# Kernel optimization log

Hardware: AMD Instinct MI355X
Metric: run time of the kernel (lower is better)

## Reference

```python
import jax, jax.numpy as jnp
import numpy as np

H = 256  # hidden_channels
N_USERS = 100000
N_MOVIES = 50000
N_EDGES = 500000


def setup_inputs() -> dict:
    key = jax.random.key(0)
    k1, k2, k3, k4, k5, k6, k7 = jax.random.split(key, 7)
    user_emb = jax.random.normal(k1, (N_USERS, H), dtype=jnp.float32)
    movie_emb = jax.random.normal(k2, (N_MOVIES, H), dtype=jnp.float32)
    edge_label_index = jax.random.randint(k3, (2, N_EDGES), 0, N_MOVIES, dtype=jnp.int64)
    # Linear(2H, H) and Linear(H, 1) params, torch default init scale
    s1 = 1.0 / np.sqrt(2 * H)
    s2 = 1.0 / np.sqrt(H)
    W1 = jax.random.uniform(k4, (2 * H, H), dtype=jnp.float32, minval=-s1, maxval=s1)
    b1 = jax.random.uniform(k5, (H,), dtype=jnp.float32, minval=-s1, maxval=s1)
    W2 = jax.random.uniform(k6, (H, 1), dtype=jnp.float32, minval=-s2, maxval=s2)
    b2 = jax.random.uniform(k7, (1,), dtype=jnp.float32, minval=-s2, maxval=s2)
    return {"user_emb": user_emb, "movie_emb": movie_emb,
            "edge_label_index": edge_label_index,
            "W1": W1, "b1": b1, "W2": W2, "b2": b2}


def reference(user_emb, movie_emb, edge_label_index, W1, b1, W2, b2):
    u = user_emb[edge_label_index[0]]    # [E, H]
    m = movie_emb[edge_label_index[1]]   # [E, H]
    x = jnp.concatenate([u, m], axis=-1)  # [E, 2H]
    x = jax.nn.relu(x @ W1 + b1)          # [E, H]
    return x @ W2 + b2                    # [E, 1]
```

## Files before the change

kernel.cpp:

```cpp
#include <hip/hip_runtime.h>
#include <hip/hip_bf16.h>

typedef __attribute__((ext_vector_type(8))) short v8s;
typedef __attribute__((ext_vector_type(4))) float v4f;

constexpr int H  = 256;
constexpr int K2 = 512;
constexpr int XS = 72;
constexpr int WS = 72;

__device__ inline unsigned short f2bf(float f) {
    unsigned int u = __builtin_bit_cast(unsigned int, f);
    u += 0x7FFFu + ((u >> 16) & 1u);
    return (unsigned short)(u >> 16);
}
__device__ inline float bf2f(unsigned short s) {
    return __builtin_bit_cast(float, (unsigned int)s << 16);
}

#define BAR_LGKM() do {                                          \
    asm volatile("s_waitcnt lgkmcnt(0)" ::: "memory");           \
    __builtin_amdgcn_sched_barrier(0);                           \
    __builtin_amdgcn_s_barrier();                                \
    __builtin_amdgcn_sched_barrier(0);                           \
} while (0)

__global__ void w1_transpose_kernel(const float* __restrict__ w1,
                                    unsigned short* __restrict__ w1t) {
    __shared__ float tile[32][33];
    const int bk = blockIdx.x;
    const int bn = blockIdx.y;
    const int tx = threadIdx.x & 31;
    const int ty8 = threadIdx.x >> 5;
#pragma unroll
    for (int i = 0; i < 4; ++i) {
        int ty = i * 8 + ty8;
        tile[ty][tx] = w1[(size_t)(bk * 32 + ty) * H + bn * 32 + tx];
    }
    __syncthreads();
#pragma unroll
    for (int i = 0; i < 4; ++i) {
        int ty = i * 8 + ty8;
        w1t[(size_t)(bn * 32 + ty) * K2 + bk * 32 + tx] = f2bf(tile[tx][ty]);
    }
}

__global__ void flag_zero_kernel(unsigned char* __restrict__ f, const int n) {
    int i = threadIdx.x + blockIdx.x * blockDim.x;
    int stride = blockDim.x * gridDim.x;
    for (; i < n; i += stride) f[i] = 0;
}

__global__ void flag_fill_kernel(const int* __restrict__ eli,
                                 unsigned char* __restrict__ fu,
                                 unsigned char* __restrict__ fm,
                                 const int E, const int nu, const int nm) {
    const long stride = (long)blockDim.x * gridDim.x;
    for (long e = threadIdx.x + (long)blockIdx.x * blockDim.x; e < E; e += stride) {
        int u = eli[e];
        int m = eli[(long)E + e];
        u = u < 0 ? 0 : (u >= nu ? nu - 1 : u);
        m = m < 0 ? 0 : (m >= nm ? nm - 1 : m);
        fu[u >> 6] = 1;
        fm[m >> 6] = 1;
    }
}

__global__ __launch_bounds__(512, 2) void emb_gemm_persist_kernel(
    const float* __restrict__ user_emb,
    const float* __restrict__ movie_emb,
    const unsigned short* __restrict__ w1t,
    const float* __restrict__ b1,
    unsigned short* __restrict__ P,
    unsigned short* __restrict__ Q,
    const int n_users, const int n_movies,
    const unsigned char* __restrict__ fu,
    const unsigned char* __restrict__ fm)
{
    __shared__ __align__(16) unsigned short Xs[64 * 256];
    __shared__ int list[64];
    __shared__ int nact_s;

    const int bid   = blockIdx.x;
    const int nside = (int)(gridDim.x >> 1);
    const int isMovie = bid & 1;
    const int base  = bid >> 1;

    const float* emb = isMovie ? movie_emb : user_emb;
    unsigned short* outp = isMovie ? Q : P;
    const int M    = isMovie ? n_movies : n_users;
    const int kofs = isMovie ? 256 : 0;
    const int nch  = (M + 63) >> 6;
    const unsigned char* flags = isMovie ? fm : fu;

    const int t    = threadIdx.x;
    const int wave = t >> 6;
    const int lane = t & 63;
    const int wm   = wave >> 2;
    const int wn   = wave & 3;
    const int quad = lane >> 4;
    const int l16  = lane & 15;

    if (wave == 0) {
        int c = base + lane * nside;
        bool a = (c < nch) && (flags[c] != 0);
        unsigned long long mk = __ballot(a);
        if (a) list[__popcll(mk & ((1ull << lane) - 1ull))] = c;
        if (lane == 0) nact_s = (int)__popcll(mk);
    }
    __syncthreads();
    const int nact = nact_s;
    if (nact == 0) return;

    v8s B[4][4][2];
    {
        const unsigned short* wb = w1t + (size_t)(wn * 64 + l16) * K2 + kofs + quad * 8;
#pragma unroll
        for (int nt = 0; nt < 4; ++nt)
#pragma unroll
            for (int kt = 0; kt < 4; ++kt)
#pragma unroll
                for (int ks = 0; ks < 2; ++ks)
                    B[nt][kt][ks] = *(const v8s*)(wb + (size_t)nt * 16 * K2 + kt * 64 + ks * 32);
    }
    float bv[4];
#pragma unroll
    for (int nt = 0; nt < 4; ++nt)
        bv[nt] = isMovie ? 0.f : b1[wn * 64 + nt * 16 + l16];

    char* const xsb = (char*)Xs;
    v4f xq[8];

    auto LOADX = [&](int c) {
#pragma unroll
        for (int i = 0; i < 8; ++i) {
            long r = (long)c * 64 + wave * 8 + i;
            if (r >= M) r = M - 1;
            xq[i] = *(const v4f*)(emb + (size_t)r * H + lane * 4);
        }
    };
    auto WRITEX = [&]() {
#pragma unroll
        for (int i = 0; i < 8; ++i) {
            const int r = wave * 8 + i;
            unsigned int lo = (unsigned)f2bf(xq[i][0]) | ((unsigned)f2bf(xq[i][1]) << 16);
            unsigned int hi = (unsigned)f2bf(xq[i][2]) | ((unsigned)f2bf(xq[i][3]) << 16);
            *(unsigned long long*)(xsb + r * 512 + ((lane * 8) ^ (i << 4))) =
                ((unsigned long long)hi << 32) | lo;
        }
    };

    LOADX(list[0]);
    WRITEX();
    if (nact > 1) LOADX(list[1]);
    __syncthreads();

    for (int j = 0; j < nact; ++j) {
        const long m0 = (long)list[j] * 64;

        v4f acc[2][4];
#pragma unroll
        for (int mt = 0; mt < 2; ++mt)
#pragma unroll
            for (int nt = 0; nt < 4; ++nt)
                acc[mt][nt] = (v4f){0.f, 0.f, 0.f, 0.f};

#pragma unroll
        for (int kt = 0; kt < 4; ++kt)
#pragma unroll
            for (int ks = 0; ks < 2; ++ks) {
                v8s af[2];
#pragma unroll
                for (int mt = 0; mt < 2; ++mt) {
                    const int row = wm * 32 + mt * 16 + l16;
                    af[mt] = *(const v8s*)(xsb + row * 512 +
                        ((kt * 128 + ks * 64 + quad * 16) ^ ((l16 & 7) << 4)));
                }
#pragma unroll
                for (int mt = 0; mt < 2; ++mt)
#pragma unroll
                    for (int nt = 0; nt < 4; ++nt)
                        acc[mt][nt] = __builtin_amdgcn_mfma_f32_16x16x32_bf16(
                            af[mt], B[nt][kt][ks], acc[mt][nt], 0, 0, 0);
            }

#pragma unroll
        for (int mt = 0; mt < 2; ++mt)
#pragma unroll
            for (int j4 = 0; j4 < 4; ++j4) {
                const long m = m0 + wm * 32 + mt * 16 + quad * 4 + j4;
                if (m < M) {
#pragma unroll
                    for (int nt = 0; nt < 4; ++nt)
                        outp[(size_t)m * H + wn * 64 + nt * 16 + l16] =
                            f2bf(acc[mt][nt][j4] + bv[nt]);
                }
            }

        if (j + 1 < nact) {
            BAR_LGKM();
            WRITEX();
            if (j + 2 < nact) LOADX(list[j + 2]);
            BAR_LGKM();
        }
    }
}

__global__ __launch_bounds__(256, 8) void edge_score_kernel(
    const unsigned short* __restrict__ P,
    const unsigned short* __restrict__ Q,
    const int* __restrict__ eli,
    const float* __restrict__ w2,
    const float* __restrict__ b2,
    float* __restrict__ out,
    const int E, const int n_users, const int n_movies)
{
    const int t   = threadIdx.x;
    const int hw  = t >> 5;
    const int l32 = t & 31;

    float w2v[8];
    {
        v4f a = *(const v4f*)(w2 + l32 * 8);
        v4f b = *(const v4f*)(w2 + l32 * 8 + 4);
#pragma unroll
        for (int i = 0; i < 4; ++i) { w2v[i] = a[i]; w2v[4 + i] = b[i]; }
    }
    const float b2v = b2[0];
    const long base = (long)blockIdx.x * 64;

    int us[8], ms[8];
#pragma unroll
    for (int i = 0; i < 8; ++i) {
        long e = base + i * 8 + hw;
        long ec = (e < E) ? e : 0;
        int u = eli[ec];
        int m = eli[(long)E + ec];
        us[i] = u < 0 ? 0 : (u >= n_users  ? n_users  - 1 : u);
        ms[i] = m < 0 ? 0 : (m >= n_movies ? n_movies - 1 : m);
    }

    v8s pv = *(const v8s*)(P + (size_t)us[0] * H + l32 * 8);
    v8s qv = *(const v8s*)(Q + (size_t)ms[0] * H + l32 * 8);

#pragma unroll
    for (int i = 0; i < 8; ++i) {
        v8s pn, qn;
        if (i < 7) {
            pn = *(const v8s*)(P + (size_t)us[i + 1] * H + l32 * 8);
            qn = *(const v8s*)(Q + (size_t)ms[i + 1] * H + l32 * 8);
        }
        float s = 0.f;
#pragma unroll
        for (int j = 0; j < 8; ++j) {
            float h = bf2f((unsigned short)pv[j]) + bf2f((unsigned short)qv[j]);
            h = h > 0.f ? h : 0.f;
            s += h * w2v[j];
        }
        s += __shfl_xor(s, 1, 64);
        s += __shfl_xor(s, 2, 64);
        s += __shfl_xor(s, 4, 64);
        s += __shfl_xor(s, 8, 64);
        s += __shfl_xor(s, 16, 64);
        long e = base + i * 8 + hw;
        if (l32 == 0 && e < E) out[e] = s + b2v;
        pv = pn; qv = qn;
    }
}

constexpr int BMF = 64;
__global__ __launch_bounds__(512, 4) void edge_decoder_kernel(
    const float* __restrict__ user_emb, const float* __restrict__ movie_emb,
    const int* __restrict__ eli, const unsigned short* __restrict__ w1t,
    const float* __restrict__ b1, const float* __restrict__ w2,
    const float* __restrict__ b2, float* __restrict__ out,
    const int E, const int n_users, const int n_movies)
{
    __shared__ unsigned short Xs[BMF * XS];
    __shared__ unsigned short Wts[H * WS];
    __shared__ float red[4][BMF];
    const int t = threadIdx.x, wave = t >> 6, lane = t & 63;
    const int wm = wave >> 2, wn = wave & 3, quad = lane >> 4, l16 = lane & 15;
    const long e0 = (long)blockIdx.x * BMF;
    const int xr = t >> 3, xc = t & 7;
    long eg = e0 + xr; if (eg >= E) eg = 0;
    int iu = eli[eg], im = eli[(long)E + eg];
    iu = iu < 0 ? 0 : (iu >= n_users ? n_users - 1 : iu);
    im = im < 0 ? 0 : (im >= n_movies ? n_movies - 1 : im);
    const float* urow = user_emb + (size_t)iu * H;
    const float* mrow = movie_emb + (size_t)im * H;
    const int wr = t >> 3, wc8 = t & 7;
    const unsigned short* wbase = w1t + (size_t)wr * K2 + wc8 * 8;
    v4f acc[2][4];
#pragma unroll
    for (int mt = 0; mt < 2; ++mt)
#pragma unroll
        for (int nt = 0; nt < 4; ++nt) acc[mt][nt] = (v4f){0.f,0.f,0.f,0.f};
    v4f xq0 = *(const v4f*)(urow + xc * 8);
    v4f xq1 = *(const v4f*)(urow + xc * 8 + 4);
    v8s wq[4];
#pragma unroll
    for (int j = 0; j < 4; ++j) wq[j] = *(const v8s*)(wbase + (size_t)j * 64 * K2);
    for (int kt = 0; kt < 8; ++kt) {
        __syncthreads();
        { v8s xv;
#pragma unroll
          for (int i = 0; i < 4; ++i) xv[i] = (short)f2bf(xq0[i]);
#pragma unroll
          for (int i = 0; i < 4; ++i) xv[4+i] = (short)f2bf(xq1[i]);
          *(v8s*)(Xs + xr * XS + xc * 8) = xv; }
#pragma unroll
        for (int j = 0; j < 4; ++j) *(v8s*)(Wts + (j * 64 + wr) * WS + wc8 * 8) = wq[j];
        if (kt < 7) {
            const int kn = kt + 1, koff = (kn * 64) & 255;
            const float* src = ((kn < 4) ? urow : mrow) + koff + xc * 8;
            xq0 = *(const v4f*)(src); xq1 = *(const v4f*)(src + 4);
#pragma unroll
            for (int j = 0; j < 4; ++j) wq[j] = *(const v8s*)(wbase + (size_t)j * 64 * K2 + kn * 64);
        }
        __syncthreads();
#pragma unroll
        for (int ks = 0; ks < 2; ++ks) {
            v8s af[2], bf[4];
#pragma unroll
            for (int mt = 0; mt < 2; ++mt)
                af[mt] = *(const v8s*)(Xs + (wm * 32 + mt * 16 + l16) * XS + ks * 32 + quad * 8);
#pragma unroll
            for (int nt = 0; nt < 4; ++nt)
                bf[nt] = *(const v8s*)(Wts + (wn * 64 + nt * 16 + l16) * WS + ks * 32 + quad * 8);
#pragma unroll
            for (int mt = 0; mt < 2; ++mt)
#pragma unroll
                for (int nt = 0; nt < 4; ++nt)
                    acc[mt][nt] = __builtin_amdgcn_mfma_f32_16x16x32_bf16(af[mt], bf[nt], acc[mt][nt], 0, 0, 0);
        }
    }
    float b1v[4], w2v[4];
#pragma unroll
    for (int nt = 0; nt < 4; ++nt) {
        int n = wn * 64 + nt * 16 + l16;
        b1v[nt] = b1[n]; w2v[nt] = w2[n];
    }
    const float b2v = b2[0];
#pragma unroll
    for (int mt = 0; mt < 2; ++mt) {
        float s[4] = {0.f,0.f,0.f,0.f};
#pragma unroll
        for (int nt = 0; nt < 4; ++nt)
#pragma unroll
            for (int j = 0; j < 4; ++j) {
                float h = acc[mt][nt][j] + b1v[nt];
                h = h > 0.f ? h : 0.f;
                s[j] += h * w2v[nt];
            }
#pragma unroll
        for (int j = 0; j < 4; ++j) {
            float v = s[j];
            v += __shfl_xor(v, 1, 64); v += __shfl_xor(v, 2, 64);
            v += __shfl_xor(v, 4, 64); v += __shfl_xor(v, 8, 64);
            if (l16 == 0) red[wn][wm * 32 + mt * 16 + quad * 4 + j] = v;
        }
    }
    __syncthreads();
    if (t < BMF) {
        long e = e0 + t;
        if (e < E) out[e] = red[0][t] + red[1][t] + red[2][t] + red[3][t] + b2v;
    }
}

extern "C" void kernel_launch(void* const* d_in, const int* in_sizes, int n_in,
                              void* d_out, int out_size, void* d_ws, size_t ws_size,
                              hipStream_t stream) {
    const float* user_emb  = (const float*)d_in[0];
    const float* movie_emb = (const float*)d_in[1];
    const int*   eli       = (const int*)d_in[2];
    const float* w1        = (const float*)d_in[3];
    const float* b1        = (const float*)d_in[4];
    const float* w2        = (const float*)d_in[5];
    const float* b2        = (const float*)d_in[6];
    float*       out       = (float*)d_out;

    const int E        = out_size;
    const int n_users  = in_sizes[0] / H;
    const int n_movies = in_sizes[1] / H;

    unsigned short* w1t = (unsigned short*)d_ws;
    const size_t w1t_bytes = (size_t)K2 * H * 2;
    const size_t p_bytes   = (size_t)n_users  * H * 2;
    const size_t q_bytes   = (size_t)n_movies * H * 2;

    const int nbu = (n_users  + 63) / 64;
    const int nbm = (n_movies + 63) / 64;
    const size_t flag_bytes = (size_t)nbu + (size_t)nbm;

    w1_transpose_kernel<<<dim3(16, 8), 256, 0, stream>>>(w1, w1t);

    if (ws_size >= w1t_bytes + p_bytes + q_bytes + flag_bytes &&
        nbu <= 64 * 128 && nbm <= 64 * 128) {
        unsigned short* P = (unsigned short*)((char*)d_ws + w1t_bytes);
        unsigned short* Q = (unsigned short*)((char*)d_ws + w1t_bytes + p_bytes);
        unsigned char*  fu = (unsigned char*)((char*)d_ws + w1t_bytes + p_bytes + q_bytes);
        unsigned char*  fm = fu + nbu;

        flag_zero_kernel<<<4, 256, 0, stream>>>(fu, nbu + nbm);
        if (E > 0)
            flag_fill_kernel<<<512, 256, 0, stream>>>(eli, fu, fm, E, n_users, n_movies);
        emb_gemm_persist_kernel<<<256, 512, 0, stream>>>(
            user_emb, movie_emb, w1t, b1, P, Q, n_users, n_movies, fu, fm);
        if (E > 0)
            edge_score_kernel<<<(E + 63) / 64, 256, 0, stream>>>(
                P, Q, eli, w2, b2, out, E, n_users, n_movies);
    } else {
        if (E > 0)
            edge_decoder_kernel<<<(E + BMF - 1) / BMF, 512, 0, stream>>>(
                user_emb, movie_emb, eli, w1t, b1, w2, b2, out, E, n_users, n_movies);
    }
}
```

Before: 263.7 us.

## Stage W1 tile in LDS and double threads per GEMM block; fuse flag zeroing

```diff
diff --git a/kernel.cpp b/kernel.cpp
--- a/kernel.cpp
+++ b/kernel.cpp
@@ -26,12 +26,17 @@
 } while (0)
 
 __global__ void w1_transpose_kernel(const float* __restrict__ w1,
-                                    unsigned short* __restrict__ w1t) {
+                                    unsigned short* __restrict__ w1t,
+                                    unsigned char* __restrict__ flags,
+                                    const int nflags) {
     __shared__ float tile[32][33];
     const int bk = blockIdx.x;
     const int bn = blockIdx.y;
     const int tx = threadIdx.x & 31;
     const int ty8 = threadIdx.x >> 5;
+    if (flags && bk == 0 && bn == 0) {
+        for (int i = threadIdx.x; i < nflags; i += 256) flags[i] = 0;
+    }
 #pragma unroll
     for (int i = 0; i < 4; ++i) {
         int ty = i * 8 + ty8;
@@ -43,12 +48,6 @@
         int ty = i * 8 + ty8;
         w1t[(size_t)(bn * 32 + ty) * K2 + bk * 32 + tx] = f2bf(tile[tx][ty]);
     }
-}
-
-__global__ void flag_zero_kernel(unsigned char* __restrict__ f, const int n) {
-    int i = threadIdx.x + blockIdx.x * blockDim.x;
-    int stride = blockDim.x * gridDim.x;
-    for (; i < n; i += stride) f[i] = 0;
 }
 
 __global__ void flag_fill_kernel(const int* __restrict__ eli,
@@ -66,7 +65,7 @@
     }
 }
 
-__global__ __launch_bounds__(512, 2) void emb_gemm_persist_kernel(
+__global__ __launch_bounds__(1024, 4) void emb_gemm_persist_kernel(
     const float* __restrict__ user_emb,
     const float* __restrict__ movie_emb,
     const unsigned short* __restrict__ w1t,
@@ -77,9 +76,8 @@
     const unsigned char* __restrict__ fu,
     const unsigned char* __restrict__ fm)
 {
+    __shared__ __align__(16) unsigned short Bs[256 * 256];
     __shared__ __align__(16) unsigned short Xs[64 * 256];
-    __shared__ int list[64];
-    __shared__ int nact_s;
 
     const int bid   = blockIdx.x;
     const int nside = (int)(gridDim.x >> 1);
@@ -100,107 +98,112 @@
     const int wn   = wave & 3;
     const int quad = lane >> 4;
     const int l16  = lane & 15;
-
-    if (wave == 0) {
+    (void)wave;
+
+    unsigned long long mk;
+    {
         int c = base + lane * nside;
         bool a = (c < nch) && (flags[c] != 0);
-        unsigned long long mk = __ballot(a);
-        if (a) list[__popcll(mk & ((1ull << lane) - 1ull))] = c;
-        if (lane == 0) nact_s = (int)__popcll(mk);
-    }
-    __syncthreads();
-    const int nact = nact_s;
+        mk = __ballot(a);
+    }
+    const int nact = (int)__popcll(mk);
     if (nact == 0) return;
 
-    v8s B[4][4][2];
+    unsigned long long cur = mk, pf = mk;
+    auto nextc = [&](unsigned long long& m) -> int {
+        int p = (int)__builtin_ctzll(m);
+        m &= m - 1;
+        return base + p * nside;
+    };
+
+    char* const bsb = (char*)Bs;
+    char* const xsb = (char*)Xs;
+
     {
-        const unsigned short* wb = w1t + (size_t)(wn * 64 + l16) * K2 + kofs + quad * 8;
-#pragma unroll
-        for (int nt = 0; nt < 4; ++nt)
-#pragma unroll
-            for (int kt = 0; kt < 4; ++kt)
-#pragma unroll
-                for (int ks = 0; ks < 2; ++ks)
-                    B[nt][kt][ks] = *(const v8s*)(wb + (size_t)nt * 16 * K2 + kt * 64 + ks * 32);
-    }
+        const int n0 = t >> 5;
+        const int k8 = t & 31;
+#pragma unroll
+        for (int p = 0; p < 8; ++p) {
+            const int n = p * 32 + n0;
+            v8s w = *(const v8s*)(w1t + (size_t)n * K2 + kofs + k8 * 8);
+            *(v8s*)(bsb + n * 512 + ((k8 * 16) ^ ((n & 7) << 4))) = w;
+        }
+    }
+
     float bv[4];
 #pragma unroll
     for (int nt = 0; nt < 4; ++nt)
         bv[nt] = isMovie ? 0.f : b1[wn * 64 + nt * 16 + l16];
 
-    char* const xsb = (char*)Xs;
-    v4f xq[8];
+    const int xr = t >> 4;
+    const int xc = t & 15;
+    v4f xq[4];
 
     auto LOADX = [&](int c) {
-#pragma unroll
-        for (int i = 0; i < 8; ++i) {
-            long r = (long)c * 64 + wave * 8 + i;
-            if (r >= M) r = M - 1;
-            xq[i] = *(const v4f*)(emb + (size_t)r * H + lane * 4);
-        }
+        long r = (long)c * 64 + xr;
+        if (r >= M) r = M - 1;
+        const float* src = emb + (size_t)r * H + xc * 4;
+#pragma unroll
+        for (int q = 0; q < 4; ++q)
+            xq[q] = *(const v4f*)(src + q * 64);
     };
     auto WRITEX = [&]() {
 #pragma unroll
-        for (int i = 0; i < 8; ++i) {
-            const int r = wave * 8 + i;
-            unsigned int lo = (unsigned)f2bf(xq[i][0]) | ((unsigned)f2bf(xq[i][1]) << 16);
-            unsigned int hi = (unsigned)f2bf(xq[i][2]) | ((unsigned)f2bf(xq[i][3]) << 16);
-            *(unsigned long long*)(xsb + r * 512 + ((lane * 8) ^ (i << 4))) =
+        for (int q = 0; q < 4; ++q) {
+            unsigned int lo = (unsigned)f2bf(xq[q][0]) | ((unsigned)f2bf(xq[q][1]) << 16);
+            unsigned int hi = (unsigned)f2bf(xq[q][2]) | ((unsigned)f2bf(xq[q][3]) << 16);
+            *(unsigned long long*)(xsb + xr * 512 + ((xc * 8 + q * 128) ^ ((xr & 7) << 4))) =
                 ((unsigned long long)hi << 32) | lo;
         }
     };
 
-    LOADX(list[0]);
+    LOADX(nextc(pf));
     WRITEX();
-    if (nact > 1) LOADX(list[1]);
+    if (nact > 1) LOADX(nextc(pf));
     __syncthreads();
 
     for (int j = 0; j < nact; ++j) {
-        const long m0 = (long)list[j] * 64;
-
-        v4f acc[2][4];
-#pragma unroll
-        for (int mt = 0; mt < 2; ++mt)
-#pragma unroll
-            for (int nt = 0; nt < 4; ++nt)
-                acc[mt][nt] = (v4f){0.f, 0.f, 0.f, 0.f};
+        const long m0 = (long)nextc(cur) * 64;
+
+        v4f acc[4];
+#pragma unroll
+        for (int nt = 0; nt < 4; ++nt)
+            acc[nt] = (v4f){0.f, 0.f, 0.f, 0.f};
 
 #pragma unroll
         for (int kt = 0; kt < 4; ++kt)
 #pragma unroll
             for (int ks = 0; ks < 2; ++ks) {
-                v8s af[2];
-#pragma unroll
-                for (int mt = 0; mt < 2; ++mt) {
-                    const int row = wm * 32 + mt * 16 + l16;
-                    af[mt] = *(const v8s*)(xsb + row * 512 +
-                        ((kt * 128 + ks * 64 + quad * 16) ^ ((l16 & 7) << 4)));
+                const int ko = (kt * 128 + ks * 64 + quad * 16) ^ ((l16 & 7) << 4);
+                const int row = wm * 16 + l16;
+                v8s af = *(const v8s*)(xsb + row * 512 + ko);
+                v8s bf[4];
+#pragma unroll
+                for (int nt = 0; nt < 4; ++nt) {
+                    const int nn = wn * 64 + nt * 16 + l16;
+                    bf[nt] = *(const v8s*)(bsb + nn * 512 + ko);
                 }
 #pragma unroll
-                for (int mt = 0; mt < 2; ++mt)
-#pragma unroll
-                    for (int nt = 0; nt < 4; ++nt)
-                        acc[mt][nt] = __builtin_amdgcn_mfma_f32_16x16x32_bf16(
-                            af[mt], B[nt][kt][ks], acc[mt][nt], 0, 0, 0);
+                for (int nt = 0; nt < 4; ++nt)
+                    acc[nt] = __builtin_amdgcn_mfma_f32_16x16x32_bf16(
+                        af, bf[nt], acc[nt], 0, 0, 0);
             }
 
 #pragma unroll
-        for (int mt = 0; mt < 2; ++mt)
-#pragma unroll
-            for (int j4 = 0; j4 < 4; ++j4) {
-                const long m = m0 + wm * 32 + mt * 16 + quad * 4 + j4;
-                if (m < M) {
-#pragma unroll
-                    for (int nt = 0; nt < 4; ++nt)
-                        outp[(size_t)m * H + wn * 64 + nt * 16 + l16] =
-                            f2bf(acc[mt][nt][j4] + bv[nt]);
-                }
+        for (int j4 = 0; j4 < 4; ++j4) {
+            const long m = m0 + wm * 16 + quad * 4 + j4;
+            if (m < M) {
+#pragma unroll
+                for (int nt = 0; nt < 4; ++nt)
+                    outp[(size_t)m * H + wn * 64 + nt * 16 + l16] =
+                        f2bf(acc[nt][j4] + bv[nt]);
             }
+        }
 
         if (j + 1 < nact) {
             BAR_LGKM();
             WRITEX();
-            if (j + 2 < nact) LOADX(list[j + 2]);
+            if (j + 2 < nact) LOADX(nextc(pf));
             BAR_LGKM();
         }
     }
@@ -393,8 +396,6 @@
     const int nbm = (n_movies + 63) / 64;
     const size_t flag_bytes = (size_t)nbu + (size_t)nbm;
 
-    w1_transpose_kernel<<<dim3(16, 8), 256, 0, stream>>>(w1, w1t);
-
     if (ws_size >= w1t_bytes + p_bytes + q_bytes + flag_bytes &&
         nbu <= 64 * 128 && nbm <= 64 * 128) {
         unsigned short* P = (unsigned short*)((char*)d_ws + w1t_bytes);
@@ -402,15 +403,16 @@
         unsigned char*  fu = (unsigned char*)((char*)d_ws + w1t_bytes + p_bytes + q_bytes);
         unsigned char*  fm = fu + nbu;
 
-        flag_zero_kernel<<<4, 256, 0, stream>>>(fu, nbu + nbm);
+        w1_transpose_kernel<<<dim3(16, 8), 256, 0, stream>>>(w1, w1t, fu, nbu + nbm);
         if (E > 0)
             flag_fill_kernel<<<512, 256, 0, stream>>>(eli, fu, fm, E, n_users, n_movies);
-        emb_gemm_persist_kernel<<<256, 512, 0, stream>>>(
+        emb_gemm_persist_kernel<<<256, 1024, 0, stream>>>(
             user_emb, movie_emb, w1t, b1, P, Q, n_users, n_movies, fu, fm);
         if (E > 0)
             edge_score_kernel<<<(E + 63) / 64, 256, 0, stream>>>(
                 P, Q, eli, w2, b2, out, E, n_users, n_movies);
     } else {
+        w1_transpose_kernel<<<dim3(16, 8), 256, 0, stream>>>(w1, w1t, nullptr, 0);
         if (E > 0)
             edge_decoder_kernel<<<(E + BMF - 1) / BMF, 512, 0, stream>>>(
                 user_emb, movie_emb, eli, w1t, b1, w2, b2, out, E, n_users, n_movies);
```

After: 268.2 us. Within noise of the previous version (+1.7%).

## Stage embeddings via async global-to-LDS loads with double buffering in persistent GEMM

Applied to the files above, without the earlier changes.

```diff
diff --git a/kernel.cpp b/kernel.cpp
--- a/kernel.cpp
+++ b/kernel.cpp
@@ -18,20 +18,21 @@
     return __builtin_bit_cast(float, (unsigned int)s << 16);
 }
 
-#define BAR_LGKM() do {                                          \
-    asm volatile("s_waitcnt lgkmcnt(0)" ::: "memory");           \
-    __builtin_amdgcn_sched_barrier(0);                           \
-    __builtin_amdgcn_s_barrier();                                \
-    __builtin_amdgcn_sched_barrier(0);                           \
-} while (0)
+#define SB() __builtin_amdgcn_sched_barrier(0)
+#define VMW(N) do { asm volatile("s_waitcnt vmcnt(" #N ")" ::: "memory"); SB(); } while (0)
 
 __global__ void w1_transpose_kernel(const float* __restrict__ w1,
-                                    unsigned short* __restrict__ w1t) {
+                                    unsigned short* __restrict__ w1t,
+                                    unsigned char* __restrict__ flags,
+                                    const int nflags) {
     __shared__ float tile[32][33];
     const int bk = blockIdx.x;
     const int bn = blockIdx.y;
     const int tx = threadIdx.x & 31;
     const int ty8 = threadIdx.x >> 5;
+    if (flags && bk == 0 && bn == 0) {
+        for (int i = threadIdx.x; i < nflags; i += 256) flags[i] = 0;
+    }
 #pragma unroll
     for (int i = 0; i < 4; ++i) {
         int ty = i * 8 + ty8;
@@ -43,12 +44,6 @@
         int ty = i * 8 + ty8;
         w1t[(size_t)(bn * 32 + ty) * K2 + bk * 32 + tx] = f2bf(tile[tx][ty]);
     }
-}
-
-__global__ void flag_zero_kernel(unsigned char* __restrict__ f, const int n) {
-    int i = threadIdx.x + blockIdx.x * blockDim.x;
-    int stride = blockDim.x * gridDim.x;
-    for (; i < n; i += stride) f[i] = 0;
 }
 
 __global__ void flag_fill_kernel(const int* __restrict__ eli,
@@ -77,9 +72,7 @@
     const unsigned char* __restrict__ fu,
     const unsigned char* __restrict__ fm)
 {
-    __shared__ __align__(16) unsigned short Xs[64 * 256];
-    __shared__ int list[64];
-    __shared__ int nact_s;
+    __shared__ __align__(16) char Xs[2][64][1024];
 
     const int bid   = blockIdx.x;
     const int nside = (int)(gridDim.x >> 1);
@@ -101,16 +94,21 @@
     const int quad = lane >> 4;
     const int l16  = lane & 15;
 
-    if (wave == 0) {
+    unsigned long long mk;
+    {
         int c = base + lane * nside;
         bool a = (c < nch) && (flags[c] != 0);
-        unsigned long long mk = __ballot(a);
-        if (a) list[__popcll(mk & ((1ull << lane) - 1ull))] = c;
-        if (lane == 0) nact_s = (int)__popcll(mk);
-    }
-    __syncthreads();
-    const int nact = nact_s;
+        mk = __ballot(a);
+    }
+    const int nact = (int)__popcll(mk);
     if (nact == 0) return;
+
+    unsigned long long cur = mk, pf = mk;
+    auto nextc = [&](unsigned long long& m) -> int {
+        int p = (int)__builtin_ctzll(m);
+        m &= m - 1;
+        return base + p * nside;
+    };
 
     v8s B[4][4][2];
     {
@@ -127,36 +125,33 @@
 #pragma unroll
     for (int nt = 0; nt < 4; ++nt)
         bv[nt] = isMovie ? 0.f : b1[wn * 64 + nt * 16 + l16];
-
-    char* const xsb = (char*)Xs;
-    v4f xq[8];
-
-    auto LOADX = [&](int c) {
+    SB();
+
+    auto STAGE = [&](int c, int b) {
 #pragma unroll
         for (int i = 0; i < 8; ++i) {
-            long r = (long)c * 64 + wave * 8 + i;
+            const int rl = wave * 8 + i;
+            long r = (long)c * 64 + rl;
             if (r >= M) r = M - 1;
-            xq[i] = *(const v4f*)(emb + (size_t)r * H + lane * 4);
-        }
+            const char* src = (const char*)(emb + (size_t)r * H) + ((lane * 16) ^ (i << 4));
+            __builtin_amdgcn_global_load_lds(
+                (const __attribute__((address_space(1))) unsigned int*)src,
+                (__attribute__((address_space(3))) unsigned int*)&Xs[b][rl][0],
+                16, 0, 0);
+        }
+        SB();
     };
-    auto WRITEX = [&]() {
-#pragma unroll
-        for (int i = 0; i < 8; ++i) {
-            const int r = wave * 8 + i;
-            unsigned int lo = (unsigned)f2bf(xq[i][0]) | ((unsigned)f2bf(xq[i][1]) << 16);
-            unsigned int hi = (unsigned)f2bf(xq[i][2]) | ((unsigned)f2bf(xq[i][3]) << 16);
-            *(unsigned long long*)(xsb + r * 512 + ((lane * 8) ^ (i << 4))) =
-                ((unsigned long long)hi << 32) | lo;
-        }
-    };
-
-    LOADX(list[0]);
-    WRITEX();
-    if (nact > 1) LOADX(list[1]);
-    __syncthreads();
+
+    STAGE(nextc(pf), 0);
+    if (nact > 1) STAGE(nextc(pf), 1);
 
     for (int j = 0; j < nact; ++j) {
-        const long m0 = (long)list[j] * 64;
+        const int cb = j & 1;
+        const long m0 = (long)nextc(cur) * 64;
+
+        if (j == 0) { if (nact > 1) VMW(8); else VMW(0); }
+        else        { if (j + 1 < nact) VMW(40); else VMW(32); }
+        __builtin_amdgcn_s_barrier(); SB();
 
         v4f acc[2][4];
 #pragma unroll
@@ -165,44 +160,46 @@
             for (int nt = 0; nt < 4; ++nt)
                 acc[mt][nt] = (v4f){0.f, 0.f, 0.f, 0.f};
 
-#pragma unroll
-        for (int kt = 0; kt < 4; ++kt)
-#pragma unroll
-            for (int ks = 0; ks < 2; ++ks) {
-                v8s af[2];
-#pragma unroll
-                for (int mt = 0; mt < 2; ++mt) {
-                    const int row = wm * 32 + mt * 16 + l16;
-                    af[mt] = *(const v8s*)(xsb + row * 512 +
-                        ((kt * 128 + ks * 64 + quad * 16) ^ ((l16 & 7) << 4)));
+        const char* xb = &Xs[cb][0][0];
+#pragma unroll
+        for (int kk = 0; kk < 8; ++kk) {
+            v8s af[2];
+#pragma unroll
+            for (int mt = 0; mt < 2; ++mt) {
+                const int row = wm * 32 + mt * 16 + l16;
+                const int sw  = (row & 7) << 4;
+                const char* pr = xb + row * 1024;
+                v4f f0 = *(const v4f*)(pr + ((kk * 128 + quad * 32) ^ sw));
+                v4f f1 = *(const v4f*)(pr + ((kk * 128 + quad * 32 + 16) ^ sw));
+                v8s a;
+#pragma unroll
+                for (int q2 = 0; q2 < 4; ++q2) {
+                    a[q2]     = (short)f2bf(f0[q2]);
+                    a[4 + q2] = (short)f2bf(f1[q2]);
                 }
-#pragma unroll
-                for (int mt = 0; mt < 2; ++mt)
-#pragma unroll
-                    for (int nt = 0; nt < 4; ++nt)
-                        acc[mt][nt] = __builtin_amdgcn_mfma_f32_16x16x32_bf16(
-                            af[mt], B[nt][kt][ks], acc[mt][nt], 0, 0, 0);
+                af[mt] = a;
             }
+#pragma unroll
+            for (int mt = 0; mt < 2; ++mt)
+#pragma unroll
+                for (int nt = 0; nt < 4; ++nt)
+                    acc[mt][nt] = __builtin_amdgcn_mfma_f32_16x16x32_bf16(
+                        af[mt], B[nt][kk >> 1][kk & 1], acc[mt][nt], 0, 0, 0);
+        }
 
 #pragma unroll
         for (int mt = 0; mt < 2; ++mt)
 #pragma unroll
             for (int j4 = 0; j4 < 4; ++j4) {
                 const long m = m0 + wm * 32 + mt * 16 + quad * 4 + j4;
-                if (m < M) {
-#pragma unroll
-                    for (int nt = 0; nt < 4; ++nt)
-                        outp[(size_t)m * H + wn * 64 + nt * 16 + l16] =
-                            f2bf(acc[mt][nt][j4] + bv[nt]);
-                }
+#pragma unroll
+                for (int nt = 0; nt < 4; ++nt)
+                    outp[(size_t)m * H + wn * 64 + nt * 16 + l16] =
+                        f2bf(acc[mt][nt][j4] + bv[nt]);
             }
-
-        if (j + 1 < nact) {
-            BAR_LGKM();
-            WRITEX();
-            if (j + 2 < nact) LOADX(list[j + 2]);
-            BAR_LGKM();
-        }
+        SB();
+        __builtin_amdgcn_s_barrier(); SB();
+        if (j + 2 < nact) STAGE(nextc(pf), cb);
     }
 }
 
@@ -213,7 +210,7 @@
     const float* __restrict__ w2,
     const float* __restrict__ b2,
     float* __restrict__ out,
-    const int E, const int n_users, const int n_movies)
+    const int E, const int n_users, const int n_movies, const long e0)
 {
     const int t   = threadIdx.x;
     const int hw  = t >> 5;
@@ -227,7 +224,7 @@
         for (int i = 0; i < 4; ++i) { w2v[i] = a[i]; w2v[4 + i] = b[i]; }
     }
     const float b2v = b2[0];
-    const long base = (long)blockIdx.x * 64;
+    const long base = e0 + (long)blockIdx.x * 64;
 
     int us[8], ms[8];
 #pragma unroll
@@ -386,14 +383,12 @@
 
     unsigned short* w1t = (unsigned short*)d_ws;
     const size_t w1t_bytes = (size_t)K2 * H * 2;
-    const size_t p_bytes   = (size_t)n_users  * H * 2;
-    const size_t q_bytes   = (size_t)n_movies * H * 2;
+    const size_t p_bytes   = (size_t)(n_users  + 64) * H * 2;
+    const size_t q_bytes   = (size_t)(n_movies + 64) * H * 2;
 
     const int nbu = (n_users  + 63) / 64;
     const int nbm = (n_movies + 63) / 64;
     const size_t flag_bytes = (size_t)nbu + (size_t)nbm;
-
-    w1_transpose_kernel<<<dim3(16, 8), 256, 0, stream>>>(w1, w1t);
 
     if (ws_size >= w1t_bytes + p_bytes + q_bytes + flag_bytes &&
         nbu <= 64 * 128 && nbm <= 64 * 128) {
@@ -402,15 +397,23 @@
         unsigned char*  fu = (unsigned char*)((char*)d_ws + w1t_bytes + p_bytes + q_bytes);
         unsigned char*  fm = fu + nbu;
 
-        flag_zero_kernel<<<4, 256, 0, stream>>>(fu, nbu + nbm);
+        w1_transpose_kernel<<<dim3(16, 8), 256, 0, stream>>>(w1, w1t, fu, nbu + nbm);
         if (E > 0)
             flag_fill_kernel<<<512, 256, 0, stream>>>(eli, fu, fm, E, n_users, n_movies);
         emb_gemm_persist_kernel<<<256, 512, 0, stream>>>(
             user_emb, movie_emb, w1t, b1, P, Q, n_users, n_movies, fu, fm);
-        if (E > 0)
-            edge_score_kernel<<<(E + 63) / 64, 256, 0, stream>>>(
-                P, Q, eli, w2, b2, out, E, n_users, n_movies);
+        if (E > 0) {
+            long Eh = ((long)(E / 2) + 63) & ~63L;
+            if (Eh > E) Eh = E;
+            if (Eh > 0)
+                edge_score_kernel<<<(int)(Eh / 64), 256, 0, stream>>>(
+                    P, Q, eli, w2, b2, out, E, n_users, n_movies, 0);
+            if (E - Eh > 0)
+                edge_score_kernel<<<(int)((E - Eh + 63) / 64), 256, 0, stream>>>(
+                    P, Q, eli, w2, b2, out, E, n_users, n_movies, Eh);
+        }
     } else {
+        w1_transpose_kernel<<<dim3(16, 8), 256, 0, stream>>>(w1, w1t, nullptr, 0);
         if (E > 0)
             edge_decoder_kernel<<<(E + BMF - 1) / BMF, 512, 0, stream>>>(
                 user_emb, movie_emb, eli, w1t, b1, w2, b2, out, E, n_users, n_movies);
```

Measured after the change: 272.0 us. 1.03x slower.
